# Kernel optimization log

Measured on AMD Instinct MI355X. Metric: run time of the kernel, lower is better.

## Reference

```python
import jax, jax.numpy as jnp
from jax import lax
import numpy as np

VOCAB, EMBED, HID = 128, 256, 1024
BATCH, SEQ = 64, 1024


def setup_inputs() -> dict:
    key = jax.random.key(0)
    ks = jax.random.split(key, 8)
    s = 0.05  # small init scale so tanh/sigmoid gates are not saturated
    return {
        "ids": jax.random.randint(ks[0], (BATCH, SEQ), 0, VOCAB, dtype=jnp.int32),
        "emb": jax.random.normal(ks[1], (VOCAB, EMBED), jnp.float32) * s,
        "w_in": jax.random.normal(ks[2], (EMBED, 3 * HID), jnp.float32) * s,
        "b_in": jnp.zeros((3 * HID,), jnp.float32),
        "w_rec": jax.random.normal(ks[3], (HID, 3 * HID), jnp.float32) * s,
        "b_rec": jnp.zeros((3 * HID,), jnp.float32),
        "w_out": jax.random.normal(ks[4], (HID, VOCAB), jnp.float32) * s,
        "b_out": jnp.zeros((VOCAB,), jnp.float32),
    }


def reference(ids, emb, w_in, b_in, w_rec, b_rec, w_out, b_out):
    # Embedding lookup: [B,T,E]
    x = emb[ids]
    # Input-side gate pre-activations computed for all timesteps at once: [B,T,3H]
    xg = x @ w_in + b_in
    B = x.shape[0]
    H = w_rec.shape[0]
    h0 = jnp.zeros((B, H), x.dtype)  # gru.get_initial_state -> zeros

    def step(h, xg_t):
        # Keras GRU, reset_after=True: recurrent bias added BEFORE reset-gate product
        rg = h @ w_rec + b_rec                      # [B,3H]
        xz, xr, xh = jnp.split(xg_t, 3, axis=-1)
        rz, rr, rh = jnp.split(rg, 3, axis=-1)
        z = jax.nn.sigmoid(xz + rz)                 # update gate
        r = jax.nn.sigmoid(xr + rr)                 # reset gate
        hh = jnp.tanh(xh + r * rh)                  # candidate
        h_new = z * h + (1.0 - z) * hh
        return h_new, h_new

    _, hs = lax.scan(step, h0, jnp.swapaxes(xg, 0, 1))  # hs: [T,B,H]
    hs = jnp.swapaxes(hs, 0, 1)                          # [B,T,H]
    logits = hs @ w_out + b_out                          # [B,T,V]
    return logits
```

## Files before the change

kernel.cpp:

```cpp
#include <hip/hip_runtime.h>
#include <hip/hip_bf16.h>
#include <hip/hip_fp16.h>
#include <cstddef>


#define VOCABN 128
#define HIDN   1024
#define BN     64
#define TN     1024
#define C3N    3072
#define NREP   2
#define FREP   3
#define NGRU   256

typedef _Float16 half8 __attribute__((ext_vector_type(8)));
typedef float    f32x4 __attribute__((ext_vector_type(4)));
typedef unsigned int u32x4 __attribute__((ext_vector_type(4)));
typedef unsigned int u32x2 __attribute__((ext_vector_type(2)));

__global__ __launch_bounds__(256, 1) void emb_gemm(
    const float* __restrict__ emb, const float* __restrict__ w_in,
    const float* __restrict__ b_in, _Float16* __restrict__ Mtab)
{
    __shared__ float se[16][256];
    const int tid = threadIdx.x;
    const int c   = blockIdx.x * 256 + tid;
    const int v0  = blockIdx.y * 16;
#pragma unroll
    for (int i = 0; i < 16; ++i) {
        int flat = i * 256 + tid;
        int r = flat >> 8, e = flat & 255;
        se[r][e] = emb[(v0 + r) * 256 + e];
    }
    __syncthreads();
    float acc[16];
#pragma unroll
    for (int r = 0; r < 16; ++r) acc[r] = 0.f;
    for (int e = 0; e < 256; ++e) {
        float w = w_in[(size_t)e * C3N + c];
#pragma unroll
        for (int r = 0; r < 16; ++r) acc[r] = fmaf(se[r][e], w, acc[r]);
    }
    float bc = b_in[c];
#pragma unroll
    for (int r = 0; r < 16; ++r)
        Mtab[(size_t)(v0 + r) * C3N + c] = (_Float16)(acc[r] + bc);
}

__global__ __launch_bounds__(256, 1) void fused_persist(
    const int* __restrict__ ids, const _Float16* __restrict__ Mtab_g,
    const float* __restrict__ w_rec, const float* __restrict__ b_rec,
    _Float16* __restrict__ comm,
    unsigned int* __restrict__ flags,
    _Float16* __restrict__ hs,
    const float* __restrict__ w_out, const float* __restrict__ b_out,
    float* __restrict__ out)
{
    __shared__ __align__(16) char smem[46080];
    _Float16* wh   = (_Float16*)smem;
    _Float16* mtab = (_Float16*)(smem + 32768);
    _Float16* sht  = (_Float16*)(smem + 45056);
    const half8* whp = (const half8*)wh;

    const int tid = threadIdx.x;

    if (blockIdx.x >= NGRU) {
        _Float16* sa = (_Float16*)smem;
        const int bid = blockIdx.x - NGRU;
        const int m0  = bid * 16;
        const int tn  = m0 >> 6;
        const int pl  = (m0 >> 4) & 3;
        if (tid < 64) {
            const unsigned int* pollp = flags + 2 * 4096 + (tid * 4 + pl) * 16;
            const unsigned int tv = (unsigned int)(tn + 1);
            while (true) {
                unsigned int f;
                asm volatile("global_load_dword %0, %1, off sc0 sc1\n\t"
                             "s_waitcnt vmcnt(0)"
                             : "=v"(f) : "v"(pollp) : "memory");
                if (__all(f >= tv)) break;
                __builtin_amdgcn_s_sleep(32);
            }
        }
        __syncthreads();
#pragma unroll
        for (int i = 0; i < 8; ++i) {
            int flat = i * 256 + tid;
            int r = flat >> 7, kc = flat & 127;
            const _Float16* p = hs + (size_t)(m0 + r) * HIDN + kc * 8;
            u32x4 hv;
            asm volatile("global_load_dword" "x4 %0, %1, off sc0 sc1\n\t"
                         "s_waitcnt vmcnt(0)"
                         : "=v"(hv) : "v"(p) : "memory");
            *(u32x4*)(sa + (size_t)r * HIDN + kc * 8) = hv;
        }
        __syncthreads();
        const int v = tid & 127, g = tid >> 7;
        float acc[8];
#pragma unroll
        for (int r = 0; r < 8; ++r) acc[r] = 0.f;
        for (int k = 0; k < 1024; ++k) {
            float wv = w_out[(size_t)k * VOCABN + v];
#pragma unroll
            for (int r = 0; r < 8; ++r)
                acc[r] = fmaf((float)sa[(size_t)(g * 8 + r) * HIDN + k], wv, acc[r]);
        }
        float bo = b_out[v];
#pragma unroll
        for (int r = 0; r < 8; ++r) {
            int m = m0 + g * 8 + r;
            out[((size_t)(m & 63) * TN + (m >> 6)) * VOCABN + v] = acc[r] + bo;
        }
        return;
    }

    if (tid >= 64) return;
    const int l  = tid;
    const int w  = blockIdx.x & 63;
    const int mt = blockIdx.x >> 6;
    const int jj = l & 15;
    const int lh = l >> 4;

    for (int i = 0; i < 256; ++i) {
        int flat = i * 64 + l;
        int e  = flat & 7;
        int ll = (flat >> 3) & 63;
        int kt = flat >> 9;
        int k   = kt * 32 + (ll >> 4) * 8 + e;
        int col = 2048 + w * 16 + (ll & 15);
        wh[(kt * 64 + ll) * 8 + e] = (_Float16)w_rec[(size_t)k * C3N + col];
    }
    for (int i = 0; i < 96; ++i) {
        int flat = i * 64 + l;
        int v = flat / 48, c = flat % 48;
        int col = (c >> 4) * 1024 + w * 16 + (c & 15);
        mtab[v * 48 + c] = Mtab_g[(size_t)v * C3N + col];
    }
    half8 wz[32], wr[32];
#pragma unroll
    for (int kt = 0; kt < 32; ++kt) {
#pragma unroll
        for (int e = 0; e < 8; ++e) {
            int k = kt * 32 + lh * 8 + e;
            wz[kt][e] = (_Float16)w_rec[(size_t)k * C3N + w * 16 + jj];
            wr[kt][e] = (_Float16)w_rec[(size_t)k * C3N + 1024 + w * 16 + jj];
        }
    }
    const float bz = b_rec[w * 16 + jj];
    const float br = b_rec[1024 + w * 16 + jj];
    const float bh = b_rec[2048 + w * 16 + jj];
    asm volatile("s_waitcnt lgkmcnt(0)" ::: "memory");
    __builtin_amdgcn_sched_barrier(0);

    const int bbase = mt * 16 + lh * 4;
    float hprev[4] = {0.f, 0.f, 0.f, 0.f};

    const int ktp = w >> 1;
    _Float16* cw_base = comm + (size_t)mt * 16384 + ktp * 512
                      + (w & 1) * 256 + l * 4;
    const _Float16* cr_base = comm + (size_t)(w & 1) * 131072
                            + (size_t)mt * 16384 + (size_t)l * 8;
    unsigned int* myflag = flags + (w * 4 + mt) * 16;
    const unsigned int* pollp = flags + (w & 1) * 4096 + (l * 4 + mt) * 16;

    int idsv[4];
#pragma unroll
    for (int q = 0; q < 4; ++q) idsv[q] = ids[(size_t)(bbase + q) * TN];

#define ISSUE(BUF, G) do { _Pragma("unroll")                                  \
    for (int i_ = 0; i_ < 8; ++i_)                                            \
        asm volatile("global_load_dwordx4 %0, %1, off sc0 sc1"                \
            : "=v"(BUF[i_]) : "v"(crd + (8*(G)+i_) * 512) : "memory");        \
    } while (0)

#define WAITN(N) do {                                                         \
    asm volatile("s_waitcnt vmcnt(" #N ")" ::: "memory");                     \
    __builtin_amdgcn_sched_barrier(0); } while (0)

#define PROCG(BUF, G) do { _Pragma("unroll")                                  \
    for (int i_ = 0; i_ < 8; ++i_) {                                          \
        half8 a_ = __builtin_bit_cast(half8, BUF[i_]);                        \
        int kt_ = 8*(G) + i_;                                                 \
        acc0 = __builtin_amdgcn_mfma_f32_16x16x32_f16(a_, wz[kt_], acc0, 0, 0, 0); \
        acc1 = __builtin_amdgcn_mfma_f32_16x16x32_f16(a_, wr[kt_], acc1, 0, 0, 0); \
        acc2 = __builtin_amdgcn_mfma_f32_16x16x32_f16(a_, whp[kt_ * 64 + l], acc2, 0, 0, 0); \
    } } while (0)

    for (int t = 0; t < TN; ++t) {
        {
            const unsigned int tv = (unsigned int)t;
            while (true) {
                unsigned int f;
                asm volatile("global_load_dword %0, %1, off sc0 sc1\n\t"
                             "s_waitcnt vmcnt(0)"
                             : "=v"(f) : "v"(pollp) : "memory");
                if (__all(f >= tv)) break;
                __builtin_amdgcn_s_sleep(1);
            }
        }
        __builtin_amdgcn_sched_barrier(0);

        const _Float16* crd = cr_base + (size_t)(t & 1) * 65536;
        u32x4 bA[8], bB[8], bC[8];
        f32x4 acc0 = {0.f, 0.f, 0.f, 0.f};
        f32x4 acc1 = {0.f, 0.f, 0.f, 0.f};
        f32x4 acc2 = {0.f, 0.f, 0.f, 0.f};

        ISSUE(bA, 0); ISSUE(bB, 1); ISSUE(bC, 2);
        WAITN(16); PROCG(bA, 0); ISSUE(bA, 3);
        WAITN(16); PROCG(bB, 1);
        WAITN(8);  PROCG(bC, 2);
        WAITN(0);  PROCG(bA, 3);

        float hnv[4];
#pragma unroll
        for (int q = 0; q < 4; ++q) {
            float az = acc0[q], ar = acc1[q], ah = acc2[q];
            int id = idsv[q];
            float xz = (float)mtab[id * 48 + jj];
            float xr = (float)mtab[id * 48 + 16 + jj];
            float xh = (float)mtab[id * 48 + 32 + jj];
            float z  = 1.f / (1.f + __expf(-(xz + az + bz)));
            float r  = 1.f / (1.f + __expf(-(xr + ar + br)));
            float hh = tanhf(xh + r * (ah + bh));
            float hn = z * hprev[q] + (1.f - z) * hh;
            hprev[q] = hn;
            hnv[q] = hn;
        }
#pragma unroll
        for (int q = 0; q < 4; ++q) {
            unsigned int hv16 = (unsigned int)__builtin_bit_cast(
                unsigned short, (_Float16)hnv[q]);
            _Float16* hp = hs + ((size_t)t * BN + (bbase + q)) * HIDN + w * 16 + jj;
            asm volatile("global_store_short %0, %1, off sc0 sc1"
                         :: "v"(hp), "v"(hv16) : "memory");
        }
#pragma unroll
        for (int q = 0; q < 4; ++q)
            sht[(lh * 4 + q) * 16 + jj] = (_Float16)hnv[q];
        asm volatile("s_waitcnt lgkmcnt(0)" ::: "memory");
        __builtin_amdgcn_sched_barrier(0);
        {
            const int B   = (l >> 1) & 15;
            const int jj0 = 8 * (l >> 5) + (l & 1) * 4;
            u32x2 pk = *(const u32x2*)&sht[B * 16 + jj0];
            _Float16* cwp = cw_base + (size_t)((t + 1) & 1) * 65536;
#pragma unroll
            for (int rr = 0; rr < NREP; ++rr)
                asm volatile("global_store_dwordx2 %0, %1, off sc0 sc1"
                             :: "v"(cwp + rr * 131072), "v"(pk) : "memory");
        }
        if (t + 1 < TN) {
#pragma unroll
            for (int q = 0; q < 4; ++q)
                idsv[q] = ids[(size_t)(bbase + q) * TN + t + 1];
            WAITN(4);
        } else {
            WAITN(0);
        }
        if (l == 0) {
            unsigned int fv = (unsigned int)(t + 1);
#pragma unroll
            for (int rr = 0; rr < FREP; ++rr)
                asm volatile("global_store_dword %0, %1, off sc0 sc1"
                             :: "v"(myflag + rr * 4096), "v"(fv) : "memory");
        }
    }
#undef ISSUE
#undef WAITN
#undef PROCG
}

extern "C" void kernel_launch(void* const* d_in, const int* in_sizes, int n_in,
                              void* d_out, int out_size, void* d_ws, size_t ws_size,
                              hipStream_t stream) {
    const int*   ids   = (const int*)d_in[0];
    const float* emb   = (const float*)d_in[1];
    const float* w_in  = (const float*)d_in[2];
    const float* b_in  = (const float*)d_in[3];
    const float* w_rec = (const float*)d_in[4];
    const float* b_rec = (const float*)d_in[5];
    const float* w_out = (const float*)d_in[6];
    const float* b_out = (const float*)d_in[7];
    float* out = (float*)d_out;

    char* ws = (char*)d_ws;
    _Float16* Mtab = (_Float16*)ws;
    size_t off = (size_t)VOCABN * C3N * 2;
    _Float16* comm = (_Float16*)(ws + off); off += (size_t)NREP * 131072 * 2;
    unsigned int* flags = (unsigned int*)(ws + off); off += FREP * 4096 * 4;
    _Float16* hs = (_Float16*)(ws + off);

    emb_gemm<<<dim3(12, 8), 256, 0, stream>>>(emb, w_in, b_in, Mtab);
    hipMemsetAsync(comm, 0, (size_t)NREP * 131072 * 2, stream);
    hipMemsetAsync(flags, 0, FREP * 4096 * 4, stream);

    fused_persist<<<NGRU + (BN * TN) / 16, 256, 0, stream>>>(
        ids, Mtab, w_rec, b_rec, comm, flags, hs, w_out, b_out, out);
}
```

Baseline: 4.684 ms.

## Make logits blocks persistent and pack hidden-state stores into dwordx2

The output-projection part of the fused kernel now launches a fixed 256 persistent blocks, each looping over 16 row tiles and polling the timestep flags per tile, instead of launching one block per tile (4096 blocks). This avoids a huge grid of blocks spinning on flags and competing with the recurrent GRU blocks for scheduling. The GRU step now writes its hidden state to hs with one packed 8-byte store per lane, reusing the shared-memory transpose already used for the comm buffer, instead of four 2-byte scalar stores. The risk is that the logits work is serialized per block, so projection tiles may lag behind the recurrence and lengthen the tail after the last step.

Result: no change. 4.654 ms (-0.6%).

```diff
diff --git a/kernel.cpp b/kernel.cpp
--- a/kernel.cpp
+++ b/kernel.cpp
@@ -12,6 +12,7 @@
 #define NREP   2
 #define FREP   3
 #define NGRU   256
+#define NLOG   256
 
 typedef _Float16 half8 __attribute__((ext_vector_type(8)));
 typedef float    f32x4 __attribute__((ext_vector_type(4)));
@@ -66,50 +67,56 @@
 
     if (blockIdx.x >= NGRU) {
         _Float16* sa = (_Float16*)smem;
-        const int bid = blockIdx.x - NGRU;
-        const int m0  = bid * 16;
-        const int tn  = m0 >> 6;
-        const int pl  = (m0 >> 4) & 3;
-        if (tid < 64) {
-            const unsigned int* pollp = flags + 2 * 4096 + (tid * 4 + pl) * 16;
-            const unsigned int tv = (unsigned int)(tn + 1);
-            while (true) {
-                unsigned int f;
-                asm volatile("global_load_dword %0, %1, off sc0 sc1\n\t"
+        const int wk = blockIdx.x - NGRU;
+        for (int i = 0; i < 16; ++i) {
+            const int tile = wk + NLOG * i;
+            const int m0   = tile * 16;
+            const int tn   = tile >> 2;
+            const int pl   = tile & 3;
+            if (tid < 64) {
+                const unsigned int* pollp =
+                    flags + 2 * 4096 + (tid * 4 + pl) * 16;
+                const unsigned int tv = (unsigned int)(tn + 1);
+                while (true) {
+                    unsigned int f;
+                    asm volatile("global_load_dword %0, %1, off sc0 sc1\n\t"
+                                 "s_waitcnt vmcnt(0)"
+                                 : "=v"(f) : "v"(pollp) : "memory");
+                    if (__all(f >= tv)) break;
+                    __builtin_amdgcn_s_sleep(64);
+                }
+            }
+            __syncthreads();
+#pragma unroll
+            for (int j = 0; j < 8; ++j) {
+                int flat = j * 256 + tid;
+                int r = flat >> 7, kc = flat & 127;
+                const _Float16* p = hs + (size_t)(m0 + r) * HIDN + kc * 8;
+                u32x4 hv;
+                asm volatile("global_load_dwordx4 %0, %1, off sc0 sc1\n\t"
                              "s_waitcnt vmcnt(0)"
-                             : "=v"(f) : "v"(pollp) : "memory");
-                if (__all(f >= tv)) break;
-                __builtin_amdgcn_s_sleep(32);
-            }
-        }
-        __syncthreads();
-#pragma unroll
-        for (int i = 0; i < 8; ++i) {
-            int flat = i * 256 + tid;
-            int r = flat >> 7, kc = flat & 127;
-            const _Float16* p = hs + (size_t)(m0 + r) * HIDN + kc * 8;
-            u32x4 hv;
-            asm volatile("global_load_dword" "x4 %0, %1, off sc0 sc1\n\t"
-                         "s_waitcnt vmcnt(0)"
-                         : "=v"(hv) : "v"(p) : "memory");
-            *(u32x4*)(sa + (size_t)r * HIDN + kc * 8) = hv;
-        }
-        __syncthreads();
-        const int v = tid & 127, g = tid >> 7;
-        float acc[8];
-#pragma unroll
-        for (int r = 0; r < 8; ++r) acc[r] = 0.f;
-        for (int k = 0; k < 1024; ++k) {
-            float wv = w_out[(size_t)k * VOCABN + v];
-#pragma unroll
-            for (int r = 0; r < 8; ++r)
-                acc[r] = fmaf((float)sa[(size_t)(g * 8 + r) * HIDN + k], wv, acc[r]);
-        }
-        float bo = b_out[v];
-#pragma unroll
-        for (int r = 0; r < 8; ++r) {
-            int m = m0 + g * 8 + r;
-            out[((size_t)(m & 63) * TN + (m >> 6)) * VOCABN + v] = acc[r] + bo;
+                             : "=v"(hv) : "v"(p) : "memory");
+                *(u32x4*)(sa + (size_t)r * HIDN + kc * 8) = hv;
+            }
+            __syncthreads();
+            const int v = tid & 127, g = tid >> 7;
+            float acc[8];
+#pragma unroll
+            for (int r = 0; r < 8; ++r) acc[r] = 0.f;
+            for (int k = 0; k < 1024; ++k) {
+                float wv = w_out[(size_t)k * VOCABN + v];
+#pragma unroll
+                for (int r = 0; r < 8; ++r)
+                    acc[r] = fmaf((float)sa[(size_t)(g * 8 + r) * HIDN + k],
+                                  wv, acc[r]);
+            }
+            float bo = b_out[v];
+#pragma unroll
+            for (int r = 0; r < 8; ++r) {
+                int m = m0 + g * 8 + r;
+                out[((size_t)(m & 63) * TN + (m >> 6)) * VOCABN + v] = acc[r] + bo;
+            }
+            __syncthreads();
         }
         return;
     }
@@ -162,6 +169,10 @@
                             + (size_t)mt * 16384 + (size_t)l * 8;
     unsigned int* myflag = flags + (w * 4 + mt) * 16;
     const unsigned int* pollp = flags + (w & 1) * 4096 + (l * 4 + mt) * 16;
+
+    const int Bq  = (l >> 1) & 15;
+    const int jq  = 8 * (l >> 5) + (l & 1) * 4;
+    _Float16* hs_base = hs + (size_t)(mt * 16 + Bq) * HIDN + w * 16 + jq;
 
     int idsv[4];
 #pragma unroll
@@ -228,22 +239,15 @@
             hnv[q] = hn;
         }
 #pragma unroll
-        for (int q = 0; q < 4; ++q) {
-            unsigned int hv16 = (unsigned int)__builtin_bit_cast(
-                unsigned short, (_Float16)hnv[q]);
-            _Float16* hp = hs + ((size_t)t * BN + (bbase + q)) * HIDN + w * 16 + jj;
-            asm volatile("global_store_short %0, %1, off sc0 sc1"
-                         :: "v"(hp), "v"(hv16) : "memory");
-        }
-#pragma unroll
         for (int q = 0; q < 4; ++q)
             sht[(lh * 4 + q) * 16 + jj] = (_Float16)hnv[q];
         asm volatile("s_waitcnt lgkmcnt(0)" ::: "memory");
         __builtin_amdgcn_sched_barrier(0);
         {
-            const int B   = (l >> 1) & 15;
-            const int jj0 = 8 * (l >> 5) + (l & 1) * 4;
-            u32x2 pk = *(const u32x2*)&sht[B * 16 + jj0];
+            u32x2 pk = *(const u32x2*)&sht[Bq * 16 + jq];
+            _Float16* hp = hs_base + (size_t)t * BN * HIDN;
+            asm volatile("global_store_dwordx2 %0, %1, off sc0 sc1"
+                         :: "v"(hp), "v"(pk) : "memory");
             _Float16* cwp = cw_base + (size_t)((t + 1) & 1) * 65536;
 #pragma unroll
             for (int rr = 0; rr < NREP; ++rr)
@@ -295,6 +299,6 @@
     hipMemsetAsync(comm, 0, (size_t)NREP * 131072 * 2, stream);
     hipMemsetAsync(flags, 0, FREP * 4096 * 4, stream);
 
-    fused_persist<<<NGRU + (BN * TN) / 16, 256, 0, stream>>>(
+    fused_persist<<<NGRU + NLOG, 256, 0, stream>>>(
         ids, Mtab, w_rec, b_rec, comm, flags, hs, w_out, b_out, out);
 }
```
